# Performance work log

Hardware: AMD Instinct MI355X
Metric: run time of the kernel (lower is better)

## Reference

```python
import jax, jax.numpy as jnp
import numpy as np

N_HEAD = 16
N_KV = 4
HEAD_DIM = 128
N_EMBD = 2048
GATE_CH = 32


def setup_inputs() -> dict:
    key = jax.random.key(0)
    ks = jax.random.split(key, 9)
    B, T = 2, 2048
    return {
        "x": jax.random.normal(ks[0], (B, T, N_EMBD), jnp.float32),
        "ve": jax.random.normal(ks[1], (B, T, N_KV * HEAD_DIM), jnp.float32),
        "cos": jax.random.uniform(ks[2], (T, 1, HEAD_DIM // 2), jnp.float32),
        "sin": jax.random.uniform(ks[3], (T, 1, HEAD_DIM // 2), jnp.float32),
        "wq": jax.random.normal(ks[4], (N_HEAD * HEAD_DIM, N_EMBD), jnp.float32) * 0.02,
        "wk": jax.random.normal(ks[5], (N_KV * HEAD_DIM, N_EMBD), jnp.float32) * 0.02,
        "wv": jax.random.normal(ks[6], (N_KV * HEAD_DIM, N_EMBD), jnp.float32) * 0.02,
        "wo": jax.random.normal(ks[7], (N_EMBD, N_EMBD), jnp.float32) * 0.02,
        "wgate": jax.random.normal(ks[8], (N_KV, GATE_CH), jnp.float32) * 0.02,
        "window_size": 512,
    }


def _rope(t, cos, sin):
    half = t.shape[-1] // 2
    t1, t2 = t[..., :half], t[..., half:]
    return jnp.concatenate([t1 * cos + t2 * sin, -t1 * sin + t2 * cos], axis=-1)


def _rms(t):
    eps = jnp.finfo(t.dtype).eps
    return t * jax.lax.rsqrt(jnp.mean(t * t, axis=-1, keepdims=True) + eps)


def reference(x, ve, cos, sin, wq, wk, wv, wo, wgate, window_size):
    B, T, _ = x.shape
    q = (x @ wq.T).reshape(B, T, N_HEAD, HEAD_DIM)
    k = (x @ wk.T).reshape(B, T, N_KV, HEAD_DIM)
    v = (x @ wv.T).reshape(B, T, N_KV, HEAD_DIM)
    # value-embedding gate
    gate = 2.0 * jax.nn.sigmoid(x[..., :GATE_CH] @ wgate.T)  # [B,T,N_KV]
    v = v + gate[..., None] * ve.reshape(B, T, N_KV, HEAD_DIM)
    # RoPE then QK RMSNorm
    q = _rms(_rope(q, cos, sin)).transpose(0, 2, 1, 3)  # [B,H,T,D]
    k = _rms(_rope(k, cos, sin)).transpose(0, 2, 1, 3)  # [B,KV,T,D]
    v = v.transpose(0, 2, 1, 3)
    rep = N_HEAD // N_KV
    k = jnp.repeat(k, rep, axis=1)  # repeat_interleave over head dim
    v = jnp.repeat(v, rep, axis=1)
    # sliding-window causal mask (past_len=0, key_len=T)
    pos = jnp.arange(T)
    mask = (pos[None, :] <= pos[:, None]) & (pos[None, :] >= pos[:, None] - window_size + 1)
    scale = 1.0 / jnp.sqrt(jnp.float32(HEAD_DIM))
    scores = jnp.einsum("bhqd,bhkd->bhqk", q, k) * scale
    scores = jnp.where(mask[None, None], scores, jnp.finfo(scores.dtype).min)
    attn = jax.nn.softmax(scores, axis=-1)
    y = jnp.einsum("bhqk,bhkd->bhqd", attn, v)
    y = y.transpose(0, 2, 1, 3).reshape(B, T, N_EMBD)
    return y @ wo.T
```

## Files before the change

kernel.cpp:

```cpp
#include <hip/hip_runtime.h>
#include <hip/hip_bf16.h>

typedef __attribute__((ext_vector_type(8))) short short8_t;
typedef __attribute__((ext_vector_type(4))) float f32x4;
typedef __attribute__((ext_vector_type(16))) float f32x16;
using bf16 = __hip_bfloat16;

#define MFMA_BF16(A, B, C) __builtin_amdgcn_mfma_f32_16x16x32_bf16((A), (B), (C), 0, 0, 0)
#define MFMA32_BF16(A, B, C) __builtin_amdgcn_mfma_f32_32x32x16_bf16((A), (B), (C), 0, 0, 0)

#define GLD_LDS16(g, l)                                                        \
  __builtin_amdgcn_global_load_lds(                                           \
      (const __attribute__((address_space(1))) unsigned int*)(const void*)(g),\
      (__attribute__((address_space(3))) unsigned int*)(void*)(l), 16, 0, 0)

__device__ __forceinline__ float bits2f(short s) {
  union { unsigned int u; float f; } c;
  c.u = ((unsigned int)(unsigned short)s) << 16;
  return c.f;
}
__device__ __forceinline__ short f2bits(float f) {
  bf16 h = __float2bfloat16(f);
  return *reinterpret_cast<short*>(&h);
}
__device__ __forceinline__ unsigned pack2(float lo, float hi) {
  return ((unsigned)(unsigned short)f2bits(lo)) |
         (((unsigned)(unsigned short)f2bits(hi)) << 16);
}
__device__ __forceinline__ float exp2_(float x) {
#if __has_builtin(__builtin_amdgcn_exp2f)
  return __builtin_amdgcn_exp2f(x);
#else
  return exp2f(x);
#endif
}

__global__ __launch_bounds__(256) void cvt_f32_bf16(const float* __restrict__ in,
                                                    short* __restrict__ out, int n) {
  int i = (blockIdx.x * 256 + threadIdx.x) * 4;
  if (i >= n) return;
  float4 v = *reinterpret_cast<const float4*>(in + i);
  short4 o;
  o.x = f2bits(v.x); o.y = f2bits(v.y); o.z = f2bits(v.z); o.w = f2bits(v.w);
  *reinterpret_cast<short4*>(out + i) = o;
}

__global__ __launch_bounds__(256) void cvt_w3(const float* __restrict__ wq,
                                              const float* __restrict__ wk,
                                              const float* __restrict__ wv,
                                              short* __restrict__ out) {
  int i = (blockIdx.x * 256 + threadIdx.x) * 4;
  const float* src;
  int off;
  if (i < 4194304) { src = wq; off = i; }
  else if (i < 5242880) { src = wk; off = i - 4194304; }
  else { src = wv; off = i - 5242880; }
  float4 v = *reinterpret_cast<const float4*>(src + off);
  short4 o;
  o.x = f2bits(v.x); o.y = f2bits(v.y); o.z = f2bits(v.z); o.w = f2bits(v.w);
  *reinterpret_cast<short4*>(out + i) = o;
}

template <int STORE_BF16>
__global__ __launch_bounds__(256, 2) void gemm_bt4(const short* __restrict__ A,
                                                   const short* __restrict__ Bt,
                                                   void* __restrict__ C,
                                                   int M, int N, int K, int NBN) {
  __shared__ __align__(16) short lds[2 * 16384];
  const int nwg = gridDim.x;
  const int cpx = nwg >> 3;
  const int wg = ((int)blockIdx.x & 7) * cpx + ((int)blockIdx.x >> 3);
  const int m0 = (wg / NBN) * 128, n0 = (wg % NBN) * 128;

  const int tid = threadIdx.x, w = tid >> 6, lane = tid & 63;
  const int wr = w >> 1, wc = w & 1;
  const int rr = lane & 15, g = lane >> 4;

  const int srow = tid >> 3;
  const int gc = (tid & 7) ^ (srow & 7);
  const short* Asrc = A + (size_t)(m0 + srow) * K + gc * 8;
  const short* Bsrc = Bt + (size_t)(n0 + srow) * K + gc * 8;
  const size_t rstep = (size_t)32 * K;
  const int dofs = tid * 16;

  const int abase = (((wr * 64 + rr) << 7) | (g << 4)) ^ ((rr & 7) << 4);
  const int bbase = ((((wc * 64 + rr) << 7) | (g << 4)) ^ ((rr & 7) << 4)) + 16384;

  f32x4 acc[4][4];
#pragma unroll
  for (int mi = 0; mi < 4; ++mi)
#pragma unroll
    for (int ni = 0; ni < 4; ++ni) acc[mi][ni] = (f32x4){0.f, 0.f, 0.f, 0.f};

  const int nt = K >> 6;

#define STAGE4(t, bufbyte) do {                                                \
    const short* a_ = Asrc + (size_t)(t) * 64;                                 \
    const short* b_ = Bsrc + (size_t)(t) * 64;                                 \
    char* la_ = (char*)lds + (bufbyte) + dofs;                                 \
    GLD_LDS16(a_,             la_);                                            \
    GLD_LDS16(a_ + rstep,     la_ + 4096);                                     \
    GLD_LDS16(a_ + 2 * rstep, la_ + 8192);                                     \
    GLD_LDS16(a_ + 3 * rstep, la_ + 12288);                                    \
    GLD_LDS16(b_,             la_ + 16384);                                    \
    GLD_LDS16(b_ + rstep,     la_ + 20480);                                    \
    GLD_LDS16(b_ + 2 * rstep, la_ + 24576);                                    \
    GLD_LDS16(b_ + 3 * rstep, la_ + 28672);                                    \
  } while (0)

  STAGE4(0, 0);
  asm volatile("s_waitcnt vmcnt(0)" ::: "memory");
  asm volatile("s_barrier" ::: "memory");

  int cur = 0;
  for (int t = 0; t < nt; ++t) {
    if (t + 1 < nt) STAGE4(t + 1, cur ^ 32768);
    const char* bufp = (const char*)lds + cur;
#pragma unroll
    for (int kk = 0; kk < 2; ++kk) {
      const int ko = kk * 64;
      short8_t a0 = *(const short8_t*)(bufp + ((abase ^ ko)));
      short8_t a1 = *(const short8_t*)(bufp + ((abase ^ ko) + 2048));
      short8_t a2 = *(const short8_t*)(bufp + ((abase ^ ko) + 4096));
      short8_t a3 = *(const short8_t*)(bufp + ((abase ^ ko) + 6144));
      short8_t b0 = *(const short8_t*)(bufp + ((bbase ^ ko)));
      short8_t b1 = *(const short8_t*)(bufp + ((bbase ^ ko) + 2048));
      short8_t b2 = *(const short8_t*)(bufp + ((bbase ^ ko) + 4096));
      short8_t b3 = *(const short8_t*)(bufp + ((bbase ^ ko) + 6144));
      __builtin_amdgcn_s_setprio(1);
      acc[0][0] = MFMA_BF16(a0, b0, acc[0][0]);
      acc[0][1] = MFMA_BF16(a0, b1, acc[0][1]);
      acc[0][2] = MFMA_BF16(a0, b2, acc[0][2]);
      acc[0][3] = MFMA_BF16(a0, b3, acc[0][3]);
      acc[1][0] = MFMA_BF16(a1, b0, acc[1][0]);
      acc[1][1] = MFMA_BF16(a1, b1, acc[1][1]);
      acc[1][2] = MFMA_BF16(a1, b2, acc[1][2]);
      acc[1][3] = MFMA_BF16(a1, b3, acc[1][3]);
      acc[2][0] = MFMA_BF16(a2, b0, acc[2][0]);
      acc[2][1] = MFMA_BF16(a2, b1, acc[2][1]);
      acc[2][2] = MFMA_BF16(a2, b2, acc[2][2]);
      acc[2][3] = MFMA_BF16(a2, b3, acc[2][3]);
      acc[3][0] = MFMA_BF16(a3, b0, acc[3][0]);
      acc[3][1] = MFMA_BF16(a3, b1, acc[3][1]);
      acc[3][2] = MFMA_BF16(a3, b2, acc[3][2]);
      acc[3][3] = MFMA_BF16(a3, b3, acc[3][3]);
      __builtin_amdgcn_s_setprio(0);
    }
    if (t + 1 < nt) {
      asm volatile("s_waitcnt vmcnt(0)" ::: "memory");
      asm volatile("s_barrier" ::: "memory");
    }
    cur ^= 32768;
  }
#undef STAGE4

#pragma unroll
  for (int mi = 0; mi < 4; ++mi)
#pragma unroll
    for (int ni = 0; ni < 4; ++ni) {
      const int row = m0 + wr * 64 + mi * 16 + g * 4;
      const int col = n0 + wc * 64 + ni * 16 + rr;
#pragma unroll
      for (int j = 0; j < 4; ++j) {
        float v = acc[mi][ni][j];
        if (STORE_BF16)
          reinterpret_cast<short*>(C)[(size_t)(row + j) * N + col] = f2bits(v);
        else
          reinterpret_cast<float*>(C)[(size_t)(row + j) * N + col] = v;
      }
    }
}

__global__ __launch_bounds__(256) void rope_rms_qk(const short* __restrict__ qkv,
                                                   const float* __restrict__ cosT,
                                                   const float* __restrict__ sinT,
                                                   short* __restrict__ qO,
                                                   short* __restrict__ kO) {
  const int T = 2048;
  int unit = blockIdx.x * 4 + (threadIdx.x >> 6);
  int lane = threadIdx.x & 63;
  int hh = unit % 20;
  int t = (unit / 20) % T;
  int b = unit / (20 * T);
  int col = hh < 16 ? hh * 128 : 2048 + (hh - 16) * 128;
  const short* src = qkv + (size_t)(b * T + t) * 3072 + col;
  float t1 = bits2f(src[lane]), t2 = bits2f(src[lane + 64]);
  float c = cosT[t * 64 + lane], s = sinT[t * 64 + lane];
  float o1 = t1 * c + t2 * s;
  float o2 = t2 * c - t1 * s;
  float ss = o1 * o1 + o2 * o2;
#pragma unroll
  for (int o = 1; o < 64; o <<= 1) ss += __shfl_xor(ss, o, 64);
  float r = rsqrtf(ss * (1.f / 128.f) + 1.1920929e-07f);
  short* dst;
  if (hh < 16) {
    r *= 0.08838834764831845f * 1.4426950408889634f;
    dst = qO + ((size_t)(b * 16 + hh) * T + t) * 128;
  } else {
    dst = kO + ((size_t)(b * 4 + (hh - 16)) * T + t) * 128;
  }
  dst[lane] = f2bits(o1 * r);
  dst[lane + 64] = f2bits(o2 * r);
}

__global__ __launch_bounds__(256) void v_gate(const short* __restrict__ qkv,
                                              const float* __restrict__ x,
                                              const float* __restrict__ ve,
                                              const float* __restrict__ wgate,
                                              short* __restrict__ vO) {
  const int T = 2048;
  int unit = blockIdx.x * 4 + (threadIdx.x >> 6);
  int lane = threadIdx.x & 63;
  int kv = unit & 3;
  int t = (unit >> 2) % T;
  int b = unit / (4 * T);
  size_t m = (size_t)b * T + t;
  float z = 0.f;
  if (lane < 32) z = x[m * 2048 + lane] * wgate[kv * 32 + lane];
#pragma unroll
  for (int o = 1; o < 64; o <<= 1) z += __shfl_xor(z, o, 64);
  float gate = 2.f / (1.f + __expf(-z));
  const short* vsrc = qkv + m * 3072 + 2560 + kv * 128;
  const float* vesrc = ve + m * 512 + kv * 128;
  short* dst = vO + ((size_t)(b * 4 + kv) * T + t) * 128;
  dst[lane] = f2bits(bits2f(vsrc[lane]) + gate * vesrc[lane]);
  dst[lane + 64] = f2bits(bits2f(vsrc[lane + 64]) + gate * vesrc[lane + 64]);
}

__global__ __launch_bounds__(256) void attn_sw2(const short* __restrict__ Q,
                                                const short* __restrict__ K,
                                                const short* __restrict__ V,
                                                short* __restrict__ Y,
                                                const int* __restrict__ winp) {
  const int T = 2048, H = 16;
  const int win = *winp;
  int combo = blockIdx.x & 7;
  int j = blockIdx.x >> 3;
  int b = combo >> 2, kvh = combo & 3;
  int h = kvh * 4 + (j & 3);
  int q0 = (j >> 2) * 128;

  __shared__ __align__(16) short Ks[64 * 128];
  __shared__ __align__(16) short Vs[128 * 64];

  int tid = threadIdx.x, w = tid >> 6, lane = tid & 63;
  int ql = lane & 31, hi = lane >> 5;
  int qrow = q0 + w * 32 + ql;

  const short* qbase = Q + ((size_t)(b * H + h) * T + qrow) * 128;
  short8_t qf[8];
#pragma unroll
  for (int ks = 0; ks < 8; ++ks)
    qf[ks] = *reinterpret_cast<const short8_t*>(qbase + ks * 16 + hi * 8);

  const short* kbase = K + (size_t)(b * 4 + kvh) * T * 128;
  const short* vbase = V + (size_t)(b * 4 + kvh) * T * 128;

  f32x16 acc[4];
#pragma unroll
  for (int dt = 0; dt < 4; ++dt)
#pragma unroll
    for (int r = 0; r < 16; ++r) acc[dt][r] = 0.f;
  float mreg = -1e30f, lsum = 0.f;

  int vkey = tid >> 2;
  int vdc = tid & 3;

  int lo = q0 - win + 1;
  if (lo < 0) lo = 0;
  lo &= ~63;
  int qmin = q0 + w * 32, qmax = qmin + 31;

  for (int kc = lo; kc < q0 + 128; kc += 64) {
    __syncthreads();
#pragma unroll
    for (int r = 0; r < 4; ++r) {
      int slot = (r * 4 + w) * 64 + lane;
      int krow = slot >> 4;
      int c16 = (slot & 15) ^ (krow & 7);
      GLD_LDS16(kbase + (size_t)(kc + krow) * 128 + c16 * 8,
                (char*)Ks + (r * 4 + w) * 1024);
    }
    {
      const short* vsrc = vbase + (size_t)(kc + vkey) * 128 + vdc * 32;
      short8_t vv[4];
#pragma unroll
      for (int q2 = 0; q2 < 4; ++q2)
        vv[q2] = *reinterpret_cast<const short8_t*>(vsrc + q2 * 8);
#pragma unroll
      for (int i = 0; i < 32; ++i) {
        int dd = vdc * 32 + i;
        int byte = dd * 128 + vkey * 2;
        byte ^= ((i & 7) ^ vdc) << 4;
        *reinterpret_cast<short*>((char*)Vs + byte) = vv[i >> 3][i & 7];
      }
    }
    __syncthreads();

    bool active = (kc <= qmax) && (kc + 63 >= qmin - win + 1);
    if (active) {
      f32x16 sA[2];
#pragma unroll
      for (int r = 0; r < 16; ++r) { sA[0][r] = 0.f; sA[1][r] = 0.f; }
#pragma unroll
      for (int kt = 0; kt < 2; ++kt) {
        int kr = kt * 32 + ql;
#pragma unroll
        for (int ks = 0; ks < 8; ++ks) {
          int byte = kr * 256 + (((ks * 2 + hi) ^ (kr & 7)) << 4);
          short8_t kf = *reinterpret_cast<const short8_t*>((char*)Ks + byte);
          sA[kt] = MFMA32_BF16(kf, qf[ks], sA[kt]);
        }
      }
      float pmax = -1e30f;
#pragma unroll
      for (int kt = 0; kt < 2; ++kt)
#pragma unroll
        for (int r = 0; r < 16; ++r) {
          int key = kc + kt * 32 + (r & 3) + 8 * (r >> 2) + 4 * hi;
          float sv = sA[kt][r];
          sv = ((unsigned)(qrow - key) < (unsigned)win) ? sv : -1e30f;
          sA[kt][r] = sv;
          pmax = fmaxf(pmax, sv);
        }
      pmax = fmaxf(pmax, __shfl_xor(pmax, 32, 64));
      float mn = fmaxf(mreg, pmax);
      float corr = exp2_(mreg - mn);
      mreg = mn;
      float rs = 0.f;
#pragma unroll
      for (int kt = 0; kt < 2; ++kt)
#pragma unroll
        for (int r = 0; r < 16; ++r) {
          float p = exp2_(sA[kt][r] - mn);
          sA[kt][r] = p;
          rs += p;
        }
      rs += __shfl_xor(rs, 32, 64);
      lsum = lsum * corr + rs;
#pragma unroll
      for (int dt = 0; dt < 4; ++dt)
#pragma unroll
        for (int r = 0; r < 16; ++r) acc[dt][r] *= corr;

#pragma unroll
      for (int kt = 0; kt < 2; ++kt)
#pragma unroll
        for (int s = 0; s < 2; ++s) {
          unsigned a = pack2(sA[kt][8 * s + 0], sA[kt][8 * s + 1]);
          unsigned bb = pack2(sA[kt][8 * s + 2], sA[kt][8 * s + 3]);
          unsigned c = pack2(sA[kt][8 * s + 4], sA[kt][8 * s + 5]);
          unsigned dd = pack2(sA[kt][8 * s + 6], sA[kt][8 * s + 7]);
          unsigned sa = __shfl_xor(a, 32, 64);
          unsigned sb = __shfl_xor(bb, 32, 64);
          unsigned sc2 = __shfl_xor(c, 32, 64);
          unsigned sd = __shfl_xor(dd, 32, 64);
          union { unsigned u[4]; short8_t s8; } pu;
          pu.u[0] = hi ? sc2 : a;
          pu.u[1] = hi ? sd : bb;
          pu.u[2] = hi ? c : sa;
          pu.u[3] = hi ? dd : sb;
          int kb = kt * 64 + s * 32 + hi * 16;
#pragma unroll
          for (int dt = 0; dt < 4; ++dt) {
            int drow = dt * 32 + ql;
            int byte = drow * 128 + kb;
            byte ^= ((drow & 7) ^ dt) << 4;
            short8_t vf = *reinterpret_cast<const short8_t*>((char*)Vs + byte);
            acc[dt] = MFMA32_BF16(vf, pu.s8, acc[dt]);
          }
        }
    }
  }

  float rinv = 1.f / lsum;
  short* ybase = Y + ((size_t)(b * T + qrow) * H + h) * 128;
#pragma unroll
  for (int dt = 0; dt < 4; ++dt)
#pragma unroll
    for (int g2 = 0; g2 < 4; ++g2) {
      short4 o;
      o.x = f2bits(acc[dt][g2 * 4 + 0] * rinv);
      o.y = f2bits(acc[dt][g2 * 4 + 1] * rinv);
      o.z = f2bits(acc[dt][g2 * 4 + 2] * rinv);
      o.w = f2bits(acc[dt][g2 * 4 + 3] * rinv);
      *reinterpret_cast<short4*>(ybase + dt * 32 + 8 * g2 + 4 * hi) = o;
    }
}

extern "C" void kernel_launch(void* const* d_in, const int* in_sizes, int n_in,
                              void* d_out, int out_size, void* d_ws, size_t ws_size,
                              hipStream_t stream) {
  const float* x = (const float*)d_in[0];
  const float* ve = (const float*)d_in[1];
  const float* cosT = (const float*)d_in[2];
  const float* sinT = (const float*)d_in[3];
  const float* wq = (const float*)d_in[4];
  const float* wk = (const float*)d_in[5];
  const float* wv = (const float*)d_in[6];
  const float* wo = (const float*)d_in[7];
  const float* wgate = (const float*)d_in[8];
  const int* winp = (const int*)d_in[9];
  float* out = (float*)d_out;
  char* ws = (char*)d_ws;

  const int B = 2, T = 2048;
  short* xb    = (short*)(ws);
  short* wqkvb = (short*)(ws + 16777216);
  short* wob   = (short*)(ws + 29360128);
  short* qkv   = (short*)(ws + 37748736);
  short* qpost = (short*)(ws + 62914560);
  short* kpost = (short*)(ws + 79691776);
  short* vpost = (short*)(ws + 83886080);
  short* ybuf  = (short*)(ws + 88080384);

  cvt_f32_bf16<<<dim3(8192), 256, 0, stream>>>(x, xb, B * T * 2048);
  cvt_w3<<<dim3(6144), 256, 0, stream>>>(wq, wk, wv, wqkvb);
  cvt_f32_bf16<<<dim3(4096), 256, 0, stream>>>(wo, wob, 2048 * 2048);

  gemm_bt4<1><<<dim3(768), 256, 0, stream>>>(xb, wqkvb, qkv, 4096, 3072, 2048, 24);

  rope_rms_qk<<<dim3(B * T * 20 / 4), 256, 0, stream>>>(qkv, cosT, sinT, qpost, kpost);
  v_gate<<<dim3(B * T), 256, 0, stream>>>(qkv, x, ve, wgate, vpost);

  attn_sw2<<<dim3(512), 256, 0, stream>>>(qpost, kpost, vpost, ybuf, winp);

  gemm_bt4<0><<<dim3(512), 256, 0, stream>>>(ybuf, wob, out, 4096, 2048, 2048, 16);
}
```

Before: 196.6 us.

## Pre-transpose V and double-buffer K/V tiles with async LDS loads in attention

Adds a separate kernel that writes V transposed (d-major) into the free qkv workspace, so the attention kernel can fetch V tiles with direct global-to-LDS loads instead of a register scatter transpose. The attention loop now double-buffers K and V in LDS, prefetching the next tile while computing the current one, using explicit vmcnt waits and barriers. Query blocks are also scheduled in reverse order so the longest-running blocks start first. The cost is one extra kernel launch plus a V round trip through memory, and twice the LDS per block, which may reduce occupancy.

After: 185.8 us. 1.06x faster.

```diff
diff --git a/kernel.cpp b/kernel.cpp
--- a/kernel.cpp
+++ b/kernel.cpp
@@ -227,9 +227,41 @@
   dst[lane + 64] = f2bits(bits2f(vsrc[lane + 64]) + gate * vesrc[lane + 64]);
 }
 
-__global__ __launch_bounds__(256) void attn_sw2(const short* __restrict__ Q,
+__global__ __launch_bounds__(256) void v_transpose(const short* __restrict__ vp,
+                                                   short* __restrict__ vT) {
+  const int T = 2048;
+  int bkv = blockIdx.x & 7;
+  int t0 = (blockIdx.x >> 3) * 64;
+  __shared__ __align__(16) short L[128 * 64];
+  int tid = threadIdx.x;
+  int tt = tid >> 2, dblk = tid & 3;
+  const short* src = vp + ((size_t)bkv * T + t0 + tt) * 128 + dblk * 32;
+  short8_t v0 = *(const short8_t*)(src);
+  short8_t v1 = *(const short8_t*)(src + 8);
+  short8_t v2 = *(const short8_t*)(src + 16);
+  short8_t v3 = *(const short8_t*)(src + 24);
+#pragma unroll
+  for (int i = 0; i < 32; ++i) {
+    int d = dblk * 32 + i;
+    int byte = (d * 128 + tt * 2) ^ ((d & 7) << 4);
+    short val = i < 8 ? v0[i] : i < 16 ? v1[i - 8] : i < 24 ? v2[i - 16] : v3[i - 24];
+    *(short*)((char*)L + byte) = val;
+  }
+  __syncthreads();
+  int d = tid >> 1, th = tid & 1;
+  short* dst = vT + ((size_t)bkv * 128 + d) * T + t0 + th * 64;
+  const char* Lp = (const char*)L;
+#pragma unroll
+  for (int g2 = 0; g2 < 4; ++g2) {
+    short8_t o = *(const short8_t*)(Lp + ((d * 128 + th * 64 + g2 * 16) ^ ((d & 7) << 4)));
+    *(short8_t*)(vT + ((size_t)bkv * 128 + d) * T + t0 + th * 32 + g2 * 8) = o;
+  }
+  (void)dst;
+}
+
+__global__ __launch_bounds__(256) void attn_sw3(const short* __restrict__ Q,
                                                 const short* __restrict__ K,
-                                                const short* __restrict__ V,
+                                                const short* __restrict__ VT,
                                                 short* __restrict__ Y,
                                                 const int* __restrict__ winp) {
   const int T = 2048, H = 16;
@@ -238,10 +270,10 @@
   int j = blockIdx.x >> 3;
   int b = combo >> 2, kvh = combo & 3;
   int h = kvh * 4 + (j & 3);
-  int q0 = (j >> 2) * 128;
-
-  __shared__ __align__(16) short Ks[64 * 128];
-  __shared__ __align__(16) short Vs[128 * 64];
+  int q0 = (15 - (j >> 2)) * 128;
+
+  __shared__ __align__(16) short Ks[2][64 * 128];
+  __shared__ __align__(16) short Vs[2][128 * 64];
 
   int tid = threadIdx.x, w = tid >> 6, lane = tid & 63;
   int ql = lane & 31, hi = lane >> 5;
@@ -254,7 +286,7 @@
     qf[ks] = *reinterpret_cast<const short8_t*>(qbase + ks * 16 + hi * 8);
 
   const short* kbase = K + (size_t)(b * 4 + kvh) * T * 128;
-  const short* vbase = V + (size_t)(b * 4 + kvh) * T * 128;
+  const short* vtbase = VT + (size_t)(b * 4 + kvh) * 128 * T;
 
   f32x16 acc[4];
 #pragma unroll
@@ -262,43 +294,50 @@
 #pragma unroll
     for (int r = 0; r < 16; ++r) acc[dt][r] = 0.f;
   float mreg = -1e30f, lsum = 0.f;
-
-  int vkey = tid >> 2;
-  int vdc = tid & 3;
 
   int lo = q0 - win + 1;
   if (lo < 0) lo = 0;
   lo &= ~63;
+  const int nt = (q0 + 128 - lo) >> 6;
   int qmin = q0 + w * 32, qmax = qmin + 31;
 
-  for (int kc = lo; kc < q0 + 128; kc += 64) {
-    __syncthreads();
-#pragma unroll
-    for (int r = 0; r < 4; ++r) {
-      int slot = (r * 4 + w) * 64 + lane;
-      int krow = slot >> 4;
-      int c16 = (slot & 15) ^ (krow & 7);
-      GLD_LDS16(kbase + (size_t)(kc + krow) * 128 + c16 * 8,
-                (char*)Ks + (r * 4 + w) * 1024);
-    }
-    {
-      const short* vsrc = vbase + (size_t)(kc + vkey) * 128 + vdc * 32;
-      short8_t vv[4];
-#pragma unroll
-      for (int q2 = 0; q2 < 4; ++q2)
-        vv[q2] = *reinterpret_cast<const short8_t*>(vsrc + q2 * 8);
-#pragma unroll
-      for (int i = 0; i < 32; ++i) {
-        int dd = vdc * 32 + i;
-        int byte = dd * 128 + vkey * 2;
-        byte ^= ((i & 7) ^ vdc) << 4;
-        *reinterpret_cast<short*>((char*)Vs + byte) = vv[i >> 3][i & 7];
-      }
-    }
-    __syncthreads();
-
+#define STAGE_A(ti, bi) do {                                                   \
+    int kc_ = lo + (ti) * 64;                                                  \
+    _Pragma("unroll")                                                          \
+    for (int r = 0; r < 4; ++r) {                                              \
+      int slot = (r * 4 + w) * 64 + lane;                                      \
+      int krow = slot >> 4;                                                    \
+      int gc = (slot & 15) ^ (krow & 7);                                       \
+      GLD_LDS16(kbase + (size_t)(kc_ + krow) * 128 + gc * 8,                   \
+                (char*)Ks[bi] + (r * 4 + w) * 1024);                           \
+    }                                                                          \
+    _Pragma("unroll")                                                          \
+    for (int r = 0; r < 4; ++r) {                                              \
+      int slot = (r * 4 + w) * 64 + lane;                                      \
+      int d_ = slot >> 3;                                                      \
+      int gc = (slot & 7) ^ (d_ & 7);                                          \
+      GLD_LDS16(vtbase + (size_t)d_ * T + kc_ + gc * 8,                        \
+                (char*)Vs[bi] + (r * 4 + w) * 1024);                           \
+    }                                                                          \
+  } while (0)
+
+  STAGE_A(0, 0);
+
+  int cur = 0;
+  for (int t = 0; t < nt; ++t) {
+    if (t + 1 < nt) {
+      STAGE_A(t + 1, cur ^ 1);
+      asm volatile("s_waitcnt vmcnt(8)" ::: "memory");
+    } else {
+      asm volatile("s_waitcnt vmcnt(0)" ::: "memory");
+    }
+    asm volatile("s_barrier" ::: "memory");
+
+    int kc = lo + t * 64;
     bool active = (kc <= qmax) && (kc + 63 >= qmin - win + 1);
     if (active) {
+      const char* Kp = (const char*)Ks[cur];
+      const char* Vp = (const char*)Vs[cur];
       f32x16 sA[2];
 #pragma unroll
       for (int r = 0; r < 16; ++r) { sA[0][r] = 0.f; sA[1][r] = 0.f; }
@@ -308,7 +347,7 @@
 #pragma unroll
         for (int ks = 0; ks < 8; ++ks) {
           int byte = kr * 256 + (((ks * 2 + hi) ^ (kr & 7)) << 4);
-          short8_t kf = *reinterpret_cast<const short8_t*>((char*)Ks + byte);
+          short8_t kf = *reinterpret_cast<const short8_t*>(Kp + byte);
           sA[kt] = MFMA32_BF16(kf, qf[ks], sA[kt]);
         }
       }
@@ -360,18 +399,20 @@
           pu.u[1] = hi ? sd : bb;
           pu.u[2] = hi ? c : sa;
           pu.u[3] = hi ? dd : sb;
-          int kb = kt * 64 + s * 32 + hi * 16;
+          const int kst = kt * 2 + s;
 #pragma unroll
           for (int dt = 0; dt < 4; ++dt) {
-            int drow = dt * 32 + ql;
-            int byte = drow * 128 + kb;
-            byte ^= ((drow & 7) ^ dt) << 4;
-            short8_t vf = *reinterpret_cast<const short8_t*>((char*)Vs + byte);
+            int d_ = dt * 32 + ql;
+            int byte = (d_ << 7) + ((((kst * 2 + hi)) ^ (d_ & 7)) << 4);
+            short8_t vf = *reinterpret_cast<const short8_t*>(Vp + byte);
             acc[dt] = MFMA32_BF16(vf, pu.s8, acc[dt]);
           }
         }
     }
+    asm volatile("s_barrier" ::: "memory");
+    cur ^= 1;
   }
+#undef STAGE_A
 
   float rinv = 1.f / lsum;
   short* ybase = Y + ((size_t)(b * T + qrow) * H + h) * 128;
@@ -413,6 +454,7 @@
   short* kpost = (short*)(ws + 79691776);
   short* vpost = (short*)(ws + 83886080);
   short* ybuf  = (short*)(ws + 88080384);
+  short* vTb   = qkv;
 
   cvt_f32_bf16<<<dim3(8192), 256, 0, stream>>>(x, xb, B * T * 2048);
   cvt_w3<<<dim3(6144), 256, 0, stream>>>(wq, wk, wv, wqkvb);
@@ -422,8 +464,9 @@
 
   rope_rms_qk<<<dim3(B * T * 20 / 4), 256, 0, stream>>>(qkv, cosT, sinT, qpost, kpost);
   v_gate<<<dim3(B * T), 256, 0, stream>>>(qkv, x, ve, wgate, vpost);
-
-  attn_sw2<<<dim3(512), 256, 0, stream>>>(qpost, kpost, vpost, ybuf, winp);
+  v_transpose<<<dim3(8 * (T / 64)), 256, 0, stream>>>(vpost, vTb);
+
+  attn_sw3<<<dim3(512), 256, 0, stream>>>(qpost, kpost, vTb, ybuf, winp);
 
   gemm_bt4<0><<<dim3(512), 256, 0, stream>>>(ybuf, wob, out, 4096, 2048, 2048, 16);
 }
```
